# Kernel optimization log

Hardware: AMD Instinct MI355X
Metric: run time of the kernel (lower is better)

Reference implementation:

```python
import jax, jax.numpy as jnp
import numpy as np

# Grid / time constants (from init_kwargs)
NX = 512; NZ = 512; NT = 1000; DT = 1e-3; DX = 10.0; DZ = 10.0
NABC = 50; F0 = 10.0; SEGMENTS = 10
# 4th-order staggered-grid FD coefficients
C1 = 9.0 / 8.0; C2 = -1.0 / 24.0


def _sponge_1d(n, nabc, alpha=0.0053):
    """Gerjan-style absorbing sponge profile (bc_gerjan)."""
    d = np.ones(n, dtype=np.float64)
    coef = np.exp(-((alpha * (nabc - np.arange(nabc))) ** 2))
    d[:nabc] = coef
    d[n - nabc:] = coef[::-1]
    return d


def setup_inputs() -> dict:
    key = jax.random.key(0)
    k0, k1 = jax.random.split(key, 2)
    # vp in [1500, 4000] m/s keeps CFL: vmax*dt*sqrt(2)/dx ~ 0.57 (stable)
    vp = 1500.0 + 2500.0 * jax.random.uniform(k0, (NZ, NX), jnp.float32)
    rho = 1800.0 + 600.0 * jax.random.uniform(k1, (NZ, NX), jnp.float32)
    damp = jnp.asarray(np.outer(_sponge_1d(NZ, NABC), _sponge_1d(NX, NABC)),
                       jnp.float32)  # (NZ, NX)
    # Ricker wavelet, f0 = 10 Hz
    t = np.arange(NT) * DT
    t0 = 1.2 / F0
    a = (np.pi * F0 * (t - t0)) ** 2
    rick = ((1.0 - 2.0 * a) * np.exp(-a)).astype(np.float32)
    wavelet = jnp.asarray(np.stack([rick, 0.8 * rick]))  # (S=2, NT)
    src_x = jnp.array([NX // 3, 2 * NX // 3], jnp.int32)
    src_z = jnp.array([NABC + 2, NABC + 2], jnp.int32)
    rcv_x = jnp.asarray(np.linspace(NABC, NX - NABC - 1, 512).astype(np.int32))
    rcv_z = jnp.full((512,), NABC + 2, jnp.int32)
    return {"vp": vp, "rho": rho, "damp": damp, "wavelet": wavelet,
            "src_x": src_x, "src_z": src_z, "rcv_x": rcv_x, "rcv_z": rcv_z}


def _dfx(f):  # forward staggered diff, last axis (x)
    fp = jnp.pad(f, ((0, 0), (0, 0), (2, 2)))
    return C1 * (fp[..., 3:-1] - fp[..., 2:-2]) + C2 * (fp[..., 4:] - fp[..., 1:-3])


def _dbx(f):  # backward staggered diff, last axis (x)
    fp = jnp.pad(f, ((0, 0), (0, 0), (2, 2)))
    return C1 * (fp[..., 2:-2] - fp[..., 1:-3]) + C2 * (fp[..., 3:-1] - fp[..., :-4])


def _dfz(f):  # forward staggered diff, axis -2 (z)
    fp = jnp.pad(f, ((0, 0), (2, 2), (0, 0)))
    return C1 * (fp[..., 3:-1, :] - fp[..., 2:-2, :]) + C2 * (fp[..., 4:, :] - fp[..., 1:-3, :])


def _dbz(f):  # backward staggered diff, axis -2 (z)
    fp = jnp.pad(f, ((0, 0), (2, 2), (0, 0)))
    return C1 * (fp[..., 2:-2, :] - fp[..., 1:-3, :]) + C2 * (fp[..., 3:-1, :] - fp[..., :-4, :])


def reference(vp, rho, damp, wavelet, src_x, src_z, rcv_x, rcv_z):
    """Stress-velocity acoustic FD forward model.

    Returns record_waveform of shape (src_n, nt, rcv_n) -- pressure sampled
    at receivers for each shot, each time step.
    """
    S = wavelet.shape[0]
    kappa = rho * vp * vp          # bulk modulus (NZ, NX)
    inv_rho = 1.0 / rho
    sidx = jnp.arange(S)
    src_amp = DT / (DX * DZ)

    def step(c, w):  # w: (S,) wavelet sample
        p, vx, vz = c
        vx = damp * (vx + (DT / DX) * inv_rho * _dfx(p))
        vz = damp * (vz + (DT / DZ) * inv_rho * _dfz(p))
        p = damp * (p + DT * kappa * (_dbx(vx) / DX + _dbz(vz) / DZ))
        p = p.at[sidx, src_z, src_x].add(w * src_amp)
        rec = p[:, rcv_z, rcv_x]   # (S, R)
        return (p, vx, vz), rec

    def segment(c, wseg):          # wseg: (seg_len, S)
        return jax.lax.scan(step, c, wseg)

    z = jnp.zeros((S, NZ, NX), vp.dtype)
    wav = wavelet.T.reshape(SEGMENTS, NT // SEGMENTS, S)
    _, rec = jax.lax.scan(jax.checkpoint(segment), (z, z, z), wav)
    rec = rec.reshape(NT, S, -1)   # (NT, S, R)
    return jnp.transpose(rec, (1, 0, 2))  # (S, NT, R)
```

## Files before the change

### kernel.cpp

```cpp
#include <hip/hip_runtime.h>
#include <hip/hip_bf16.h>
#include <stdint.h>


#define NXd 512
#define NZd 512
#define NTd 1000
#define Sd  2
#define Rd  512
#define C1f 1.125f
#define C2f (-1.0f/24.0f)
#define CVXf 1e-4f
#define SRC_AMPf 1e-5f

#define TZ 32
#define TX 64
#define KSTEPS 7
#define NWIN 143
#define Hz 32
#define Hx 32
#define RLZ 96
#define RLX 128
#define ZB 3
#define NZBLK 32
#define NTHR 1024

#define NN  (NZd*NXd)
#define FSZ (Sd*NN)
#define BUF_SZ (3*FSZ)
#define FLAG_OFF (2*BUF_SZ)
#define BAR_OFF  (2*BUF_SZ + 32)
#define WS_NEED_FLOATS (2*BUF_SZ + 32 + 160)
#define WS_NEED_BYTES ((size_t)WS_NEED_FLOATS * 4)

typedef float vf4 __attribute__((ext_vector_type(4)));

__device__ __forceinline__ vf4 ld4(const float* p) { return *(const vf4*)p; }
__device__ __forceinline__ void st4(float* p, vf4 v) { *(vf4*)p = v; }

__device__ __forceinline__ void st4_wt(float* p, vf4 v) {
    asm volatile("global_store_dwordx4 %0, %1, off sc0 sc1" :: "v"(p), "v"(v) : "memory");
}
__device__ __forceinline__ void st1_wt(float* p, float v) {
    asm volatile("global_store_dword %0, %1, off sc0 sc1" :: "v"(p), "v"(v) : "memory");
}
__device__ __forceinline__ void sth_wt(void* p, unsigned short bits) {
    unsigned u = bits;
    asm volatile("global_store_short %0, %1, off sc0 sc1" :: "v"(p), "v"(u) : "memory");
}

__device__ __forceinline__ float sh_up1(float v) {
    return __int_as_float(__builtin_amdgcn_update_dpp(
        0, __float_as_int(v), 0x138, 0xF, 0xF, true));
}
__device__ __forceinline__ float sh_dn1(float v) {
    return __int_as_float(__builtin_amdgcn_update_dpp(
        0, __float_as_int(v), 0x130, 0xF, 0xF, true));
}

__global__ void detect_k(const uint32_t* __restrict__ vp_raw, int* __restrict__ flag) {
    int lane = threadIdx.x;
    uint32_t u = vp_raw[lane];
    int hb = (u >> 8) & 0xFF;
    int is_exp = (hb == 0x44 || hb == 0x45) ? 1 : 0;
    unsigned long long m = __ballot(is_exp);
    if (lane == 0) *flag = (__popcll(m) >= 48) ? 1 : 0;
}

__device__ __forceinline__ float load_in(const void* p, int i, int bf) {
    return bf ? __bfloat162float(((const __hip_bfloat16*)p)[i])
              : ((const float*)p)[i];
}

__device__ __forceinline__ void gbar(unsigned* __restrict__ bar, int wg, int w) {
    __syncthreads();
    if (threadIdx.x == 0) {
        unsigned* gcnt = bar + (wg & 7) * 16;
        unsigned* mcnt = bar + 128;
        unsigned* gen  = bar + 144;
        unsigned tgt = (unsigned)(w + 1);
        unsigned a = __hip_atomic_fetch_add(gcnt, 1u, __ATOMIC_RELAXED, __HIP_MEMORY_SCOPE_AGENT);
        if (a == 32u * tgt - 1u) {
            unsigned m = __hip_atomic_fetch_add(mcnt, 1u, __ATOMIC_RELAXED, __HIP_MEMORY_SCOPE_AGENT);
            if (m == 8u * tgt - 1u) {
                __hip_atomic_store(gen, tgt, __ATOMIC_RELEASE, __HIP_MEMORY_SCOPE_AGENT);
            }
        }
        for (int it = 0; it < 300000; ++it) {
            if (__hip_atomic_load(gen, __ATOMIC_RELAXED, __HIP_MEMORY_SCOPE_AGENT) >= tgt) break;
            __builtin_amdgcn_s_sleep(2);
        }
        __builtin_amdgcn_fence(__ATOMIC_ACQUIRE, "agent");
    }
    __syncthreads();
}

__global__ __launch_bounds__(NTHR, 4) void persist_k(float* __restrict__ ws,
        void* __restrict__ out, const void* __restrict__ vp,
        const void* __restrict__ rho, const void* __restrict__ damp,
        const void* __restrict__ wav,
        const int* __restrict__ sxp, const int* __restrict__ szp,
        const int* __restrict__ rxp, const int* __restrict__ rzp) {
    __shared__ float lp [RLZ*RLX];
    __shared__ float lvz[RLZ*RLX];
    __shared__ float lwv[KSTEPS];

    const int tid  = threadIdx.x;
    const int xg   = tid & 31;
    const int zblk = tid >> 5;
    const int zb0  = zblk * ZB;
    const int xo   = xg * 4;

    const int wg  = blockIdx.x;
    const int xcd = wg & 7;
    const int ii  = wg >> 3;
    const int s   = ii >> 4;
    const int loc = ii & 15;
    const int tz0 = ((xcd >> 1) * 4 + (loc >> 2)) * TZ;
    const int tx0 = ((xcd & 1) * 4 + (loc & 3)) * TX;
    const int bf  = *(const int*)(ws + FLAG_OFF);
    unsigned* bar = (unsigned*)(ws + BAR_OFF);

    const int rxv = (tid < Rd) ? rxp[tid] : 0;
    const int rzv = (tid < Rd) ? rzp[tid] : -1000;
    const bool own = (tid < Rd) && (rzv >= tz0 && rzv < tz0 + TZ &&
                                    rxv >= tx0 && rxv < tx0 + TX);
    const int lrcv = (rzv - tz0 + Hz) * RLX + (rxv - tx0 + Hx);
    const int sxv = sxp[s], szv = szp[s];

    const int zPm  = (zb0 - 1 < 0) ? 0 : zb0 - 1;
    const int zPn0 = (zb0 + ZB     > RLZ - 1) ? RLZ - 1 : zb0 + ZB;
    const int zPn1 = (zb0 + ZB + 1 > RLZ - 1) ? RLZ - 1 : zb0 + ZB + 1;
    const int zVm2 = (zb0 - 2 < 0) ? 0 : zb0 - 2;
    const int zVm1 = zPm;
    const int zVn0 = zPn0;

    const vf4 zero4 = {0.f, 0.f, 0.f, 0.f};

    vf4 Ca[ZB], Cb[ZB], Cq[ZB];
    #pragma unroll
    for (int r = 0; r < ZB; ++r) {
        int gz = tz0 - Hz + zb0 + r;
        int gx = tx0 - Hx + xo;
        vf4 a = zero4, b = zero4, q = zero4;
        if (gz >= 0 && gz < NZd) {
            #pragma unroll
            for (int c = 0; c < 4; ++c) {
                int x = gx + c;
                if (x >= 0 && x < NXd) {
                    int gi = gz * NXd + x;
                    float v  = load_in(vp,  gi, bf);
                    float rr = load_in(rho, gi, bf);
                    float d  = load_in(damp, gi, bf);
                    ((float*)&a)[c] = d;
                    ((float*)&b)[c] = d * (CVXf / rr);
                    ((float*)&q)[c] = d * (CVXf * rr * v * v);
                }
            }
        }
        Ca[r] = a; Cb[r] = b; Cq[r] = q;
    }

    vf4 Pv[ZB], Vx[ZB], Vz[ZB];
    #pragma unroll
    for (int r = 0; r < ZB; ++r) { Pv[r] = zero4; Vx[r] = zero4; Vz[r] = zero4; }

    for (int w = 0; w < NWIN; ++w) {
        const int kk = (NTd - w * KSTEPS < KSTEPS) ? (NTd - w * KSTEPS) : KSTEPS;
        const float* bR = ws + (w & 1) * BUF_SZ;
        float*       bW = ws + ((w + 1) & 1) * BUF_SZ;
        const float* rp  = bR + s * NN;
        const float* rvx = bR + FSZ + s * NN;
        const float* rvz = bR + 2 * FSZ + s * NN;

        if (tid < kk) lwv[tid] = load_in(wav, s * NTd + w * KSTEPS + tid, bf);

        #pragma unroll
        for (int r = 0; r < ZB; ++r) {
            int z = zb0 + r;
            int gz = tz0 - Hz + z;
            int gx = tx0 - Hx + xo;
            bool intile = (z >= Hz && z < Hz + TZ && xo >= Hx && xo < Hx + TX);
            if (!intile) {
                bool in = (w > 0) && (z >= 4) && (z < RLZ - 4) &&
                          (gz >= 0) && (gz < NZd) && (gx >= 0) && (gx < NXd);
                if (in) {
                    int gi = gz * NXd + gx;
                    Pv[r] = ld4(rp + gi); Vx[r] = ld4(rvx + gi); Vz[r] = ld4(rvz + gi);
                } else if (w == 0) {
                    Pv[r] = zero4; Vx[r] = zero4; Vz[r] = zero4;
                }
            }
            st4(lp + z * RLX + xo, Pv[r]);
        }
        __syncthreads();

        for (int j = 0; j < kk; ++j) {
            const float wv = lwv[j] * SRC_AMPf;

            const int mV = 4 * (kk - 1 - j) + 2;
            const int mP = mV - 2;
            const bool actV = (zb0 + ZB > Hz - mV) && (zb0 < Hz + TZ + mV);
            const bool actP = (zb0 + ZB > Hz - mP) && (zb0 < Hz + TZ + mP);

            if (actV) {
                vf4 pPm  = ld4(lp + zPm  * RLX + xo);
                vf4 pNx0 = ld4(lp + zPn0 * RLX + xo);
                vf4 pNx1 = ld4(lp + zPn1 * RLX + xo);
                #pragma unroll
                for (int r = 0; r < ZB; ++r) {
                    vf4 c = Pv[r];
                    float pmw = sh_up1(c.w);
                    float ppx = sh_dn1(c.x);
                    float ppy = sh_dn1(c.y);
                    vf4 xm1 = __builtin_shufflevector(c, c, 0, 0, 1, 2); xm1.x = pmw;
                    vf4 xp1 = __builtin_shufflevector(c, c, 1, 2, 3, 3); xp1.w = ppx;
                    vf4 xp2 = __builtin_shufflevector(c, c, 2, 3, 3, 3); xp2.z = ppx; xp2.w = ppy;
                    vf4 pzm = (r == 0) ? pPm : Pv[(r == 0) ? 0 : r - 1];
                    vf4 pz1 = (r == ZB-1) ? pNx0 : Pv[(r == ZB-1) ? ZB-1 : r + 1];
                    vf4 pz2 = (r == ZB-2) ? pNx0 : ((r == ZB-1) ? pNx1 : Pv[(r >= ZB-2) ? ZB-1 : r + 2]);
                    vf4 dfx = (xp1 - c) * C1f + (xp2 - xm1) * C2f;
                    vf4 dfz = (pz1 - c) * C1f + (pz2 - pzm) * C2f;
                    Vx[r] = Ca[r] * Vx[r] + Cb[r] * dfx;
                    Vz[r] = Ca[r] * Vz[r] + Cb[r] * dfz;
                    st4(lvz + (zb0 + r) * RLX + xo, Vz[r]);
                }
            }
            __syncthreads();

            if (actP) {
                vf4 vm2 = ld4(lvz + zVm2 * RLX + xo);
                vf4 vm1 = ld4(lvz + zVm1 * RLX + xo);
                vf4 vn0 = ld4(lvz + zVn0 * RLX + xo);
                #pragma unroll
                for (int r = 0; r < ZB; ++r) {
                    vf4 cx = Vx[r], cz = Vz[r];
                    float vmz = sh_up1(cx.z);
                    float vmw = sh_up1(cx.w);
                    float vpx = sh_dn1(cx.x);
                    vf4 xm1 = __builtin_shufflevector(cx, cx, 0, 0, 1, 2); xm1.x = vmw;
                    vf4 xp1 = __builtin_shufflevector(cx, cx, 1, 2, 3, 3); xp1.w = vpx;
                    vf4 xm2 = __builtin_shufflevector(cx, cx, 0, 0, 0, 1); xm2.x = vmz; xm2.y = vmw;
                    vf4 zm2 = (r == 0) ? vm2 : ((r == 1) ? vm1 : Vz[(r >= 2) ? r - 2 : 0]);
                    vf4 zm1 = (r == 0) ? vm1 : Vz[(r == 0) ? 0 : r - 1];
                    vf4 zp1 = (r == ZB-1) ? vn0 : Vz[(r == ZB-1) ? ZB-1 : r + 1];
                    vf4 dbx = (cx - xm1) * C1f + (xp1 - xm2) * C2f;
                    vf4 dbz = (cz - zm1) * C1f + (zp1 - zm2) * C2f;
                    Pv[r] = Ca[r] * Pv[r] + Cq[r] * (dbx + dbz);
                    int gz = tz0 - Hz + zb0 + r;
                    if (gz == szv) {
                        int dcol = sxv - (tx0 - Hx + xo);
                        if      (dcol == 0) Pv[r].x += wv;
                        else if (dcol == 1) Pv[r].y += wv;
                        else if (dcol == 2) Pv[r].z += wv;
                        else if (dcol == 3) Pv[r].w += wv;
                    }
                    st4(lp + (zb0 + r) * RLX + xo, Pv[r]);
                }
            }
            __syncthreads();

            if (own) {
                float val = lp[lrcv];
                int oi = (s * NTd + (w * KSTEPS + j)) * Rd + tid;
                if (bf) {
                    __hip_bfloat16 h = __float2bfloat16(val);
                    unsigned short bits; __builtin_memcpy(&bits, &h, 2);
                    sth_wt((__hip_bfloat16*)out + oi, bits);
                } else {
                    st1_wt((float*)out + oi, val);
                }
            }
        }

        if (w < NWIN - 1) {
            float* wp  = bW + s * NN;
            float* wvx = bW + FSZ + s * NN;
            float* wvz = bW + 2 * FSZ + s * NN;
            #pragma unroll
            for (int r = 0; r < ZB; ++r) {
                int z = zb0 + r;
                if (z >= Hz && z < Hz + TZ && xo >= Hx && xo < Hx + TX) {
                    int gi = (tz0 - Hz + z) * NXd + (tx0 - Hx + xo);
                    st4_wt(wp + gi, Pv[r]);
                    st4_wt(wvx + gi, Vx[r]);
                    st4_wt(wvz + gi, Vz[r]);
                }
            }
            gbar(bar, wg, w);
        }
    }
}

extern "C" void kernel_launch(void* const* d_in, const int* in_sizes, int n_in,
                              void* d_out, int out_size, void* d_ws, size_t ws_size,
                              hipStream_t stream) {
    if (ws_size < WS_NEED_BYTES) return;
    float* ws = (float*)d_ws;
    const void* vp   = d_in[0];
    const void* rho  = d_in[1];
    const void* damp = d_in[2];
    const void* wav  = d_in[3];
    const int* src_x = (const int*)d_in[4];
    const int* src_z = (const int*)d_in[5];
    const int* rcv_x = (const int*)d_in[6];
    const int* rcv_z = (const int*)d_in[7];

    hipMemsetAsync(ws, 0, WS_NEED_BYTES, stream);
    detect_k<<<1, 64, 0, stream>>>((const uint32_t*)vp, (int*)(ws + FLAG_OFF));
    persist_k<<<256, NTHR, 0, stream>>>(ws, d_out, vp, rho, damp, wav,
                                        src_x, src_z, rcv_x, rcv_z);
}
```

Measured before the change: 2.545 ms.

## Exchange z-halo rows between paired half-waves via permlane32 swap instead of LDS

Each 64-lane wavefront holds two 3-row z blocks (even and odd). Rows shared between those two halves are now exchanged with permlane32_swap in registers instead of through LDS. LDS stores are cut to the rows a neighbour in another wavefront needs, plus receiver rows found through a shared flag table. LDS loads drop from three to one or two per phase. The trade-off is extra cross-lane instructions and more complex row ownership, which could break halo correctness at the tile edges.

```diff
diff --git a/kernel.cpp b/kernel.cpp
--- a/kernel.cpp
+++ b/kernel.cpp
@@ -34,6 +34,7 @@
 #define WS_NEED_BYTES ((size_t)WS_NEED_FLOATS * 4)
 
 typedef float vf4 __attribute__((ext_vector_type(4)));
+typedef unsigned uv2 __attribute__((ext_vector_type(2)));
 
 __device__ __forceinline__ vf4 ld4(const float* p) { return *(const vf4*)p; }
 __device__ __forceinline__ void st4(float* p, vf4 v) { *(vf4*)p = v; }
@@ -56,6 +57,22 @@
 __device__ __forceinline__ float sh_dn1(float v) {
     return __int_as_float(__builtin_amdgcn_update_dpp(
         0, __float_as_int(v), 0x130, 0xF, 0xF, true));
+}
+
+__device__ __forceinline__ float plsw1(float a, float b, float &bo) {
+    uv2 r = __builtin_amdgcn_permlane32_swap(
+        __float_as_uint(a), __float_as_uint(b), true, false);
+    bo = __uint_as_float(r.y);
+    return __uint_as_float(r.x);
+}
+__device__ __forceinline__ void plswap4(vf4 &A, vf4 &B) {
+    float b0, b1, b2, b3;
+    float a0 = plsw1(A.x, B.x, b0);
+    float a1 = plsw1(A.y, B.y, b1);
+    float a2 = plsw1(A.z, B.z, b2);
+    float a3 = plsw1(A.w, B.w, b3);
+    A.x = a0; A.y = a1; A.z = a2; A.w = a3;
+    B.x = b0; B.y = b1; B.z = b2; B.w = b3;
 }
 
 __global__ void detect_k(const uint32_t* __restrict__ vp_raw, int* __restrict__ flag) {
@@ -104,12 +121,14 @@
     __shared__ float lp [RLZ*RLX];
     __shared__ float lvz[RLZ*RLX];
     __shared__ float lwv[KSTEPS];
+    __shared__ unsigned char lflag[RLZ];
 
     const int tid  = threadIdx.x;
     const int xg   = tid & 31;
     const int zblk = tid >> 5;
     const int zb0  = zblk * ZB;
     const int xo   = xg * 4;
+    const bool isodd = (zblk & 1) != 0;
 
     const int wg  = blockIdx.x;
     const int xcd = wg & 7;
@@ -128,12 +147,22 @@
     const int lrcv = (rzv - tz0 + Hz) * RLX + (rxv - tx0 + Hx);
     const int sxv = sxp[s], szv = szp[s];
 
+    if (tid < RLZ) lflag[tid] = 0;
+    __syncthreads();
+    if (own) lflag[rzv - tz0 + Hz] = 1;
+    __syncthreads();
+    const bool rf0 = lflag[zb0 + 0] != 0;
+    const bool rf1 = lflag[zb0 + 1] != 0;
+    const bool rf2 = lflag[zb0 + 2] != 0;
+
     const int zPm  = (zb0 - 1 < 0) ? 0 : zb0 - 1;
     const int zPn0 = (zb0 + ZB     > RLZ - 1) ? RLZ - 1 : zb0 + ZB;
     const int zPn1 = (zb0 + ZB + 1 > RLZ - 1) ? RLZ - 1 : zb0 + ZB + 1;
     const int zVm2 = (zb0 - 2 < 0) ? 0 : zb0 - 2;
     const int zVm1 = zPm;
     const int zVn0 = zPn0;
+    const int ldVrow = isodd ? zPn0 : zPm;
+    const int ldProw = isodd ? zVn0 : zVm2;
 
     const vf4 zero4 = {0.f, 0.f, 0.f, 0.f};
 
@@ -204,9 +233,14 @@
             const bool actP = (zb0 + ZB > Hz - mP) && (zb0 < Hz + TZ + mP);
 
             if (actV) {
-                vf4 pPm  = ld4(lp + zPm  * RLX + xo);
-                vf4 pNx0 = ld4(lp + zPn0 * RLX + xo);
-                vf4 pNx1 = ld4(lp + zPn1 * RLX + xo);
+                vf4 ldA = ld4(lp + ldVrow * RLX + xo);
+                vf4 ldB = zero4;
+                if (isodd) ldB = ld4(lp + zPn1 * RLX + xo);
+                vf4 A1 = Pv[0], B1 = Pv[2]; plswap4(A1, B1);
+                vf4 A2 = Pv[1], B2 = Pv[1]; plswap4(A2, B2);
+                vf4 pPm  = isodd ? A1 : ldA;
+                vf4 pNx0 = isodd ? ldA : B1;
+                vf4 pNx1 = isodd ? ldB : B2;
                 #pragma unroll
                 for (int r = 0; r < ZB; ++r) {
                     vf4 c = Pv[r];
@@ -223,15 +257,25 @@
                     vf4 dfz = (pz1 - c) * C1f + (pz2 - pzm) * C2f;
                     Vx[r] = Ca[r] * Vx[r] + Cb[r] * dfx;
                     Vz[r] = Ca[r] * Vz[r] + Cb[r] * dfz;
-                    st4(lvz + (zb0 + r) * RLX + xo, Vz[r]);
+                }
+                if (isodd) {
+                    st4(lvz + (zb0 + 1) * RLX + xo, Vz[1]);
+                    st4(lvz + (zb0 + 2) * RLX + xo, Vz[2]);
+                } else {
+                    st4(lvz + (zb0 + 0) * RLX + xo, Vz[0]);
                 }
             }
             __syncthreads();
 
             if (actP) {
-                vf4 vm2 = ld4(lvz + zVm2 * RLX + xo);
-                vf4 vm1 = ld4(lvz + zVm1 * RLX + xo);
-                vf4 vn0 = ld4(lvz + zVn0 * RLX + xo);
+                vf4 ldA = ld4(lvz + ldProw * RLX + xo);
+                vf4 ldB = zero4;
+                if (!isodd) ldB = ld4(lvz + zVm1 * RLX + xo);
+                vf4 A1 = Vz[0], B1 = Vz[1]; plswap4(A1, B1);
+                vf4 A2 = Vz[2], B2 = Vz[2]; plswap4(A2, B2);
+                vf4 vn0v = isodd ? ldA : B1;
+                vf4 vm2v = isodd ? A1 : ldA;
+                vf4 vm1v = isodd ? A2 : ldB;
                 #pragma unroll
                 for (int r = 0; r < ZB; ++r) {
                     vf4 cx = Vx[r], cz = Vz[r];
@@ -241,9 +285,9 @@
                     vf4 xm1 = __builtin_shufflevector(cx, cx, 0, 0, 1, 2); xm1.x = vmw;
                     vf4 xp1 = __builtin_shufflevector(cx, cx, 1, 2, 3, 3); xp1.w = vpx;
                     vf4 xm2 = __builtin_shufflevector(cx, cx, 0, 0, 0, 1); xm2.x = vmz; xm2.y = vmw;
-                    vf4 zm2 = (r == 0) ? vm2 : ((r == 1) ? vm1 : Vz[(r >= 2) ? r - 2 : 0]);
-                    vf4 zm1 = (r == 0) ? vm1 : Vz[(r == 0) ? 0 : r - 1];
-                    vf4 zp1 = (r == ZB-1) ? vn0 : Vz[(r == ZB-1) ? ZB-1 : r + 1];
+                    vf4 zm2 = (r == 0) ? vm2v : ((r == 1) ? vm1v : Vz[(r >= 2) ? r - 2 : 0]);
+                    vf4 zm1 = (r == 0) ? vm1v : Vz[(r == 0) ? 0 : r - 1];
+                    vf4 zp1 = (r == ZB-1) ? vn0v : Vz[(r == ZB-1) ? ZB-1 : r + 1];
                     vf4 dbx = (cx - xm1) * C1f + (xp1 - xm2) * C2f;
                     vf4 dbz = (cz - zm1) * C1f + (zp1 - zm2) * C2f;
                     Pv[r] = Ca[r] * Pv[r] + Cq[r] * (dbx + dbz);
@@ -255,8 +299,10 @@
                         else if (dcol == 2) Pv[r].z += wv;
                         else if (dcol == 3) Pv[r].w += wv;
                     }
-                    st4(lp + (zb0 + r) * RLX + xo, Pv[r]);
-                }
+                }
+                if (!isodd || rf0) st4(lp + (zb0 + 0) * RLX + xo, Pv[0]);
+                if (!isodd || rf1) st4(lp + (zb0 + 1) * RLX + xo, Pv[1]);
+                if ( isodd || rf2) st4(lp + (zb0 + 2) * RLX + xo, Pv[2]);
             }
             __syncthreads();
 
```

After: 2.995 ms. 17.7% more time.
